# Kernel tuning notes

Hardware: AMD Instinct MI355X
Metric: run time of the kernel (lower is better)

Reference implementation:

```python
import jax, jax.numpy as jnp
import numpy as np
import math

NQ, NK, QDIM, MDIM, VDIM = 8192, 8192, 512, 512, 512
NEG = -float(1 << 32)


def setup_inputs() -> dict:
    key = jax.random.key(0)
    ks = jax.random.split(key, 8)
    Q = jax.random.normal(ks[0], (NQ, QDIM), dtype=jnp.float32)
    K = jax.random.normal(ks[1], (NK, QDIM), dtype=jnp.float32)
    V = jax.random.normal(ks[2], (NK, VDIM), dtype=jnp.float32)
    mask = jax.random.randint(ks[3], (NQ, NK), 0, 2) == 1
    s = 1.0 / math.sqrt(QDIM)
    WQ_w = jax.random.uniform(ks[4], (MDIM, QDIM), minval=-s, maxval=s, dtype=jnp.float32)
    WQ_b = jax.random.uniform(ks[5], (MDIM,), minval=-s, maxval=s, dtype=jnp.float32)
    WK_w = jax.random.uniform(ks[6], (MDIM, QDIM), minval=-s, maxval=s, dtype=jnp.float32)
    WK_b = jax.random.uniform(ks[7], (MDIM,), minval=-s, maxval=s, dtype=jnp.float32)
    return {"Q": Q, "K": K, "V": V, "WQ_w": WQ_w, "WQ_b": WQ_b,
            "WK_w": WK_w, "WK_b": WK_b, "mask": mask}


def reference(Q, K, V, WQ_w, WQ_b, WK_w, WK_b, mask):
    # Linear projections: y = x @ W^T + b
    Qp = Q @ WQ_w.T + WQ_b          # [NQ, MDIM]
    Kp = K @ WK_w.T + WK_b          # [NK, MDIM]
    scale = 1.0 / math.sqrt(MDIM)
    attn = (Qp @ Kp.T) * scale      # [NQ, NK]
    attn = jnp.where(mask, NEG, attn)
    attn = jax.nn.softmax(attn, axis=-1)
    return attn @ V                 # [NQ, VDIM]
```

## Files before the change

kernel.cpp:

```cpp
#include <hip/hip_runtime.h>

typedef __attribute__((ext_vector_type(8))) short short8;
typedef __attribute__((ext_vector_type(4))) float f32x4;

#define DEVFN __device__ __forceinline__

constexpr float NEGF = -4294967296.0f;
constexpr float SCALE_LOG2E = 0.06375872f;

DEVFN unsigned short f2bf(float f) {
  unsigned int u = __float_as_uint(f);
  u += 0x7FFFu + ((u >> 16) & 1u);
  return (unsigned short)(u >> 16);
}
DEVFN float bf2f(unsigned short h) { return __uint_as_float((unsigned)h << 16); }

DEVFN float exp2v(float x) {
  float r;
  asm("v_exp_f32 %0, %1" : "=v"(r) : "v"(x));
  return r;
}

DEVFN void gl_lds16(const void* g, void* l) {
  __builtin_amdgcn_global_load_lds(
      (const __attribute__((address_space(1))) unsigned int*)g,
      (__attribute__((address_space(3))) unsigned int*)l, 16, 0, 0);
}

DEVFN float dpp_fmax16(float x) {
  int v;
  v = __builtin_amdgcn_update_dpp(0, __float_as_int(x), 0xB1, 0xF, 0xF, true);
  x = fmaxf(x, __int_as_float(v));
  v = __builtin_amdgcn_update_dpp(0, __float_as_int(x), 0x4E, 0xF, 0xF, true);
  x = fmaxf(x, __int_as_float(v));
  v = __builtin_amdgcn_update_dpp(0, __float_as_int(x), 0x141, 0xF, 0xF, true);
  x = fmaxf(x, __int_as_float(v));
  v = __builtin_amdgcn_update_dpp(0, __float_as_int(x), 0x140, 0xF, 0xF, true);
  x = fmaxf(x, __int_as_float(v));
  return x;
}
DEVFN float dpp_fadd16(float x) {
  int v;
  v = __builtin_amdgcn_update_dpp(0, __float_as_int(x), 0xB1, 0xF, 0xF, true);
  x += __int_as_float(v);
  v = __builtin_amdgcn_update_dpp(0, __float_as_int(x), 0x4E, 0xF, 0xF, true);
  x += __int_as_float(v);
  v = __builtin_amdgcn_update_dpp(0, __float_as_int(x), 0x141, 0xF, 0xF, true);
  x += __int_as_float(v);
  v = __builtin_amdgcn_update_dpp(0, __float_as_int(x), 0x140, 0xF, 0xF, true);
  x += __int_as_float(v);
  return x;
}

__global__ void k_detect(const unsigned int* __restrict__ q, const unsigned int* __restrict__ m,
                         int* __restrict__ fflag, int* __restrict__ esize) {
  int lane = threadIdx.x;
  if (blockIdx.x == 0) {
    unsigned bad = 0;
    for (int i = 0; i < 64; i++) {
      unsigned v = q[i * 64 + lane];
      unsigned h = v & 0xFFFFu;
      unsigned e = (h >> 7) & 0xFFu;
      if (h != 0u && (e < 96u || e > 150u)) bad = 1;
    }
    unsigned long long anyb = __ballot(bad != 0);
    if (lane == 0) *fflag = (anyb == 0ULL) ? 1 : 0;
  } else {
    unsigned okd = 1, okh = 1, okb = 1;
    for (int i = 0; i < 64; i++) {
      unsigned v = m[i * 64 + lane];
      if (v > 1u && v != 0x3F800000u) okd = 0;
      unsigned h0 = v & 0xFFFFu, h1 = v >> 16;
      if ((h0 && h0 != 0x3F80u && h0 != 1u) || (h1 && h1 != 0x3F80u && h1 != 1u)) okh = 0;
      if (v & 0xFEFEFEFEu) okb = 0;
    }
    okd = (__ballot(okd == 0) == 0ULL);
    okh = (__ballot(okh == 0) == 0ULL);
    okb = (__ballot(okb == 0) == 0ULL);
    if (lane == 0) *esize = okd ? 4 : (okh ? 2 : 1);
  }
}

__global__ void k_prep(const void* __restrict__ Q, unsigned short* __restrict__ Qb,
                       const void* __restrict__ K, unsigned short* __restrict__ Kb,
                       const void* __restrict__ Wq, unsigned short* __restrict__ Wqb,
                       const void* __restrict__ Wk, unsigned short* __restrict__ Wkb,
                       const void* __restrict__ bq, unsigned short* __restrict__ bqb,
                       const void* __restrict__ bk, unsigned short* __restrict__ bkb,
                       const int* __restrict__ bf16flag) {
  int blk = blockIdx.x;
  const void* src; unsigned short* dst; int base, n;
  if (blk < 2048)      { src = Q;  dst = Qb;  base = blk;        n = 8192 * 512; }
  else if (blk < 4096) { src = K;  dst = Kb;  base = blk - 2048; n = 8192 * 512; }
  else if (blk < 4224) { src = Wq; dst = Wqb; base = blk - 4096; n = 512 * 512; }
  else if (blk < 4352) { src = Wk; dst = Wkb; base = blk - 4224; n = 512 * 512; }
  else if (blk == 4352){ src = bq; dst = bqb; base = 0;          n = 512; }
  else                 { src = bk; dst = bkb; base = 0;          n = 512; }
  int i = (base * 256 + threadIdx.x) * 8;
  if (i >= n) return;
  if (*bf16flag) {
    *(uint4*)(dst + i) = *(const uint4*)((const unsigned short*)src + i);
  } else {
    const float* f = (const float*)src + i;
    float4 a = *(const float4*)f, b = *(const float4*)(f + 4);
    uint4 o;
    o.x = (unsigned)f2bf(a.x) | ((unsigned)f2bf(a.y) << 16);
    o.y = (unsigned)f2bf(a.z) | ((unsigned)f2bf(a.w) << 16);
    o.z = (unsigned)f2bf(b.x) | ((unsigned)f2bf(b.y) << 16);
    o.w = (unsigned)f2bf(b.z) | ((unsigned)f2bf(b.w) << 16);
    *(uint4*)(dst + i) = o;
  }
}

__global__ void k_transpose_v(const void* __restrict__ Vsrc, const int* __restrict__ bf16flag,
                              unsigned short* __restrict__ Vt) {
  __shared__ unsigned short T[64][72];
  int t = threadIdx.x;
  int rb = blockIdx.x, cb = blockIdx.y;
  int r = t >> 3, c8 = (t & 7) * 8;
  int isbf = *bf16flag;
#pragma unroll
  for (int j = 0; j < 2; j++) {
    int row = rb * 64 + j * 32 + r;
    unsigned short e[8];
    if (isbf) {
      alignas(16) unsigned short tmp[8];
      *(uint4*)tmp = *(const uint4*)((const unsigned short*)Vsrc + (size_t)row * 512 + cb * 64 + c8);
#pragma unroll
      for (int i = 0; i < 8; i++) e[i] = tmp[i];
    } else {
      const float* f = (const float*)Vsrc + (size_t)row * 512 + cb * 64 + c8;
      float4 a = *(const float4*)f, b = *(const float4*)(f + 4);
      e[0] = f2bf(a.x); e[1] = f2bf(a.y); e[2] = f2bf(a.z); e[3] = f2bf(a.w);
      e[4] = f2bf(b.x); e[5] = f2bf(b.y); e[6] = f2bf(b.z); e[7] = f2bf(b.w);
    }
#pragma unroll
    for (int i = 0; i < 8; i++) T[c8 + i][j * 32 + r] = e[i];
  }
  __syncthreads();
#pragma unroll
  for (int j = 0; j < 2; j++) {
    int d = cb * 64 + j * 32 + r;
    alignas(16) unsigned short o[8];
#pragma unroll
    for (int i = 0; i < 8; i++) o[i] = T[j * 32 + r][c8 + i];
    int tt = rb * 2 + (c8 >> 5);
    *(uint4*)(Vt + ((size_t)tt * 512 + d) * 32 + (c8 & 31)) = *(const uint4*)o;
  }
}

DEVFN unsigned nib4(unsigned v) {
  unsigned t = v; t |= t >> 1; t |= t >> 2; t |= t >> 4; t &= 0x01010101u;
  return (t * 0x10204080u) >> 28;
}
DEVFN unsigned pair2(unsigned v) {
  unsigned t = v; t |= t >> 8; t |= t >> 4; t |= t >> 2; t |= t >> 1;
  return (t & 1u) | (((t >> 16) & 1u) << 1);
}
__global__ void k_pack(const void* __restrict__ mask, const int* __restrict__ esize,
                       unsigned long long* __restrict__ bits) {
  int wv = (blockIdx.x * blockDim.x + threadIdx.x) >> 6;
  int lane = threadIdx.x & 63;
  int sz = *esize;
  if (sz == 4) {
    const unsigned int* m = (const unsigned int*)mask;
    for (int g = wv; g < 262144; g += 4096) {
      size_t base = (size_t)g * 256 + lane;
      unsigned v0 = m[base], v1 = m[base + 64], v2 = m[base + 128], v3 = m[base + 192];
      unsigned long long b0 = __ballot(v0 != 0u);
      unsigned long long b1 = __ballot(v1 != 0u);
      unsigned long long b2 = __ballot(v2 != 0u);
      unsigned long long b3 = __ballot(v3 != 0u);
      if (lane == 0) {
        bits[g * 4 + 0] = b0; bits[g * 4 + 1] = b1;
        bits[g * 4 + 2] = b2; bits[g * 4 + 3] = b3;
      }
    }
  } else if (sz == 2) {
    const uint4* m = (const uint4*)mask;
    for (int g = wv; g < 131072; g += 4096) {
      uint4 v = m[(size_t)g * 64 + lane];
      unsigned c8 = pair2(v.x) | (pair2(v.y) << 2) | (pair2(v.z) << 4) | (pair2(v.w) << 6);
      unsigned long long x = (unsigned long long)c8 << ((lane & 7) * 8);
      x |= __shfl_xor(x, 1); x |= __shfl_xor(x, 2); x |= __shfl_xor(x, 4);
      if ((lane & 7) == 0) bits[g * 8 + (lane >> 3)] = x;
    }
  } else {
    const uint4* m = (const uint4*)mask;
    for (int g = wv; g < 65536; g += 4096) {
      uint4 v = m[(size_t)g * 64 + lane];
      unsigned c16 = nib4(v.x) | (nib4(v.y) << 4) | (nib4(v.z) << 8) | (nib4(v.w) << 12);
      unsigned long long x = (unsigned long long)c16 << ((lane & 3) * 16);
      x |= __shfl_xor(x, 1); x |= __shfl_xor(x, 2);
      if ((lane & 3) == 0) bits[g * 16 + (lane >> 2)] = x;
    }
  }
}

__global__ __launch_bounds__(256, 2) void k_proj(
    const unsigned short* __restrict__ Aq, const unsigned short* __restrict__ Wq,
    const unsigned short* __restrict__ bq, unsigned short* __restrict__ outq,
    const unsigned short* __restrict__ Ak, const unsigned short* __restrict__ Wk,
    const unsigned short* __restrict__ bk, unsigned short* __restrict__ outk) {
  const unsigned short* A = blockIdx.z ? Ak : Aq;
  const unsigned short* W = blockIdx.z ? Wk : Wq;
  const unsigned short* bias = blockIdx.z ? bk : bq;
  unsigned short* out = blockIdx.z ? outk : outq;
  float sc = blockIdx.z ? 1.0f : SCALE_LOG2E;

  __shared__ alignas(16) unsigned short As[128 * 64];
  __shared__ alignas(16) unsigned short Bs[128 * 64];
  int tid = threadIdx.x, lane = tid & 63, wave = tid >> 6;
  int wi = wave >> 1, wj = wave & 1;
  int l15 = lane & 15, l4 = lane >> 4;
  int rowbase = blockIdx.x * 128, colbase = blockIdx.y * 128;
  f32x4 acc[4][4];
#pragma unroll
  for (int i = 0; i < 4; i++)
#pragma unroll
    for (int j = 0; j < 4; j++) acc[i][j] = f32x4{0.f, 0.f, 0.f, 0.f};

  int swr = l15 & 7;
  for (int kb = 0; kb < 512; kb += 64) {
    __syncthreads();
#pragma unroll
    for (int t = 0; t < 4; t++) {
      int inst = wave * 4 + t;
      int r = inst * 8 + (lane >> 3);
      int c = ((lane & 7) ^ (r & 7)) * 8;
      gl_lds16(A + (size_t)(rowbase + r) * 512 + kb + c, &As[inst * 512]);
      gl_lds16(W + (size_t)(colbase + r) * 512 + kb + c, &Bs[inst * 512]);
    }
    __syncthreads();
#pragma unroll
    for (int t2 = 0; t2 < 2; t2++) {
      short8 a[4], b[4];
#pragma unroll
      for (int i = 0; i < 4; i++) {
        int row = wi * 64 + i * 16 + l15;
        a[i] = *(const short8*)&As[row * 64 + (((t2 * 4 + l4) ^ swr) * 8)];
      }
#pragma unroll
      for (int j = 0; j < 4; j++) {
        int row = wj * 64 + j * 16 + l15;
        b[j] = *(const short8*)&Bs[row * 64 + (((t2 * 4 + l4) ^ swr) * 8)];
      }
#pragma unroll
      for (int i = 0; i < 4; i++)
#pragma unroll
        for (int j = 0; j < 4; j++)
          acc[i][j] = __builtin_amdgcn_mfma_f32_16x16x32_bf16(a[i], b[j], acc[i][j], 0, 0, 0);
    }
  }
#pragma unroll
  for (int j = 0; j < 4; j++) {
    int col = colbase + wj * 64 + j * 16 + l15;
    float bj = bf2f(bias[col]);
#pragma unroll
    for (int i = 0; i < 4; i++) {
      int row0 = rowbase + wi * 64 + i * 16 + l4 * 4;
#pragma unroll
      for (int r = 0; r < 4; r++)
        out[(size_t)(row0 + r) * 512 + col] = f2bf((acc[i][j][r] + bj) * sc);
    }
  }
}

__global__ __launch_bounds__(512, 2) void k_attn(
    const unsigned short* __restrict__ Qp, const unsigned short* __restrict__ Kp,
    const unsigned short* __restrict__ Vt, const unsigned long long* __restrict__ mbits,
    unsigned short* __restrict__ Opart, float* __restrict__ mpart, float* __restrict__ lpart) {
  __shared__ alignas(16) unsigned short KB[2][16384];
  __shared__ alignas(16) unsigned short VB[16384];
  __shared__ alignas(16) unsigned short P2[2][4][128][8];
  __shared__ alignas(16) float alds[2][128];
  __shared__ alignas(16) int nfl[2][8];
  int tid = threadIdx.x, lane = tid & 63, wave = tid >> 6;
  int l15 = lane & 15, l4 = lane >> 4;
  int b = blockIdx.x;
  int split = b & 7;
  int qb = (b >> 3) * 128;

  short8 qf[16];
  {
    int row = qb + wave * 16 + l15;
#pragma unroll
    for (int t = 0; t < 16; t++)
      qf[t] = *(const short8*)(Qp + (size_t)row * 512 + t * 32 + l4 * 8);
  }
  f32x4 o[8][4];
#pragma unroll
  for (int i = 0; i < 8; i++)
#pragma unroll
    for (int j = 0; j < 4; j++) o[i][j] = f32x4{0.f, 0.f, 0.f, 0.f};
  float mi[4] = {NEGF, NEGF, NEGF, NEGF};
  float li_l[4] = {0.f, 0.f, 0.f, 0.f};

  int swK = l15 | ((l15 & 3) << 4);
  const unsigned int* mb32 = (const unsigned int*)mbits;

#define STAGE_K(TV, BUF)                                                         \
  {                                                                              \
    _Pragma("unroll") for (int t = 0; t < 4; t++) {                              \
      int r = wave * 4 + t;                                                      \
      int swz = (r & 15) | ((r & 3) << 4);                                       \
      gl_lds16(Kp + (size_t)((TV) * 32 + r) * 512 + ((lane ^ swz) * 8),          \
               &KB[BUF][r * 512]);                                               \
    }                                                                            \
  }
#define STAGE_V(TV)                                                              \
  {                                                                              \
    _Pragma("unroll") for (int t = 0; t < 4; t++) {                              \
      int inst = wave * 4 + t;                                                   \
      int d = inst * 16 + (lane >> 2);                                           \
      int cg = (lane & 3) ^ ((d >> 2) & 3);                                      \
      gl_lds16(Vt + (size_t)(TV) * 16384 + d * 32 + cg * 8, &VB[inst * 512]);    \
    }                                                                            \
  }
#define LOAD_MASKS(IT)                                                           \
  _Pragma("unroll") for (int r = 0; r < 4; r++)                                  \
    mw[r] = mb32[((size_t)(qb + wave * 16 + l4 * 4 + r) * 128 + split * 16 +     \
                  ((IT) >> 1)) * 2 + ((IT) & 1)];
#define QKT(BUF)                                                                 \
  {                                                                              \
    _Pragma("unroll") for (int c = 0; c < 2; c++) sacc[c] = f32x4{0.f,0.f,0.f,0.f}; \
    __builtin_amdgcn_s_setprio(1);                                               \
    _Pragma("unroll") for (int t2 = 0; t2 < 16; t2++) {                          \
      short8 a = qf[t2];                                                         \
      _Pragma("unroll") for (int c = 0; c < 2; c++) {                            \
        int row = c * 16 + l15;                                                  \
        short8 bb = *(const short8*)&KB[BUF][row * 512 + (((t2 * 4 + l4) ^ swK) * 8)]; \
        sacc[c] = __builtin_amdgcn_mfma_f32_16x16x32_bf16(a, bb, sacc[c], 0, 0, 0); \
      }                                                                          \
    }                                                                            \
    __builtin_amdgcn_s_setprio(0);                                               \
  }
#define MASK_APPLY()                                                             \
  _Pragma("unroll") for (int c = 0; c < 2; c++)                                  \
    _Pragma("unroll") for (int r = 0; r < 4; r++) {                              \
      bool msk = (mw[r] >> (c * 16 + l15)) & 1u;                                 \
      sacc[c][r] = msk ? NEGF : sacc[c][r];                                      \
    }

  STAGE_K(split * 32, 0);
  __builtin_amdgcn_s_waitcnt(0x0F70);
  __builtin_amdgcn_s_barrier();

  {
    const int tv = split * 32;
    unsigned mw[4];
    LOAD_MASKS(0);
    STAGE_K(tv + 1, 1);
    f32x4 sacc[2];
    QKT(0);
    MASK_APPLY();
    float al4[4];
    bool need = false;
#pragma unroll
    for (int r = 0; r < 4; r++) {
      float t = dpp_fmax16(fmaxf(sacc[0][r], sacc[1][r]));
      al4[r] = t;
      need |= (t > mi[r] + 11.5f);
    }
    unsigned long long blt = __ballot(need);
    if (lane == 0) nfl[0][wave] = (blt != 0ULL) ? 1 : 0;
    if (blt) {
#pragma unroll
      for (int r = 0; r < 4; r++) {
        float mn = fmaxf(mi[r], al4[r]);
        float a = exp2v(mi[r] - mn);
        li_l[r] *= a;
        mi[r] = mn;
        al4[r] = a;
      }
    } else {
#pragma unroll
      for (int r = 0; r < 4; r++) al4[r] = 1.0f;
    }
    if (l15 == 0) *(f32x4*)&alds[0][wave * 16 + l4 * 4] = f32x4{al4[0], al4[1], al4[2], al4[3]};
#pragma unroll
    for (int r = 0; r < 4; r++) {
      sacc[0][r] = exp2v(sacc[0][r] - mi[r]);
      sacc[1][r] = exp2v(sacc[1][r] - mi[r]);
      li_l[r] += sacc[0][r] + sacc[1][r];
    }
#pragma unroll
    for (int r = 0; r < 4; r++) {
      int prow = wave * 16 + l4 * 4 + r;
#pragma unroll
      for (int c = 0; c < 2; c++)
        P2[0][c * 2 + (l15 >> 3)][prow][l15 & 7] = f2bf(sacc[c][r]);
    }
    STAGE_V(tv);
    __builtin_amdgcn_s_waitcnt(0x0074);
    __builtin_amdgcn_s_barrier();
  }

  for (int it = 1; it < 32; ++it) {
    const int cur = it & 1, prv = cur ^ 1;
    const int tv = split * 32 + it;

    unsigned mw[4];
    LOAD_MASKS(it);
    STAGE_K((it < 31) ? tv + 1 : tv, prv);

    f32x4 sacc[2];
    QKT(cur);
    MASK_APPLY();

    __builtin_amdgcn_s_waitcnt(0x0F78);
    __builtin_amdgcn_sched_barrier(0);

    {
      const int4* n4 = (const int4*)&nfl[prv][0];
      int4 na = n4[0], nb4 = n4[1];
      if (na.x | na.y | na.z | na.w | nb4.x | nb4.y | nb4.z | nb4.w) {
#pragma unroll
        for (int rf = 0; rf < 8; rf++) {
          f32x4 av = *(const f32x4*)&alds[prv][rf * 16 + l4 * 4];
#pragma unroll
          for (int df = 0; df < 4; df++)
#pragma unroll
            for (int j = 0; j < 4; j++) o[rf][df][j] *= av[j];
        }
      }
    }
    short8 vf[4];
#pragma unroll
    for (int df = 0; df < 4; df++) {
      int d = wave * 64 + df * 16 + l15;
      vf[df] = *(const short8*)&VB[d * 32 + ((l4 ^ ((l15 >> 2) & 3)) * 8)];
    }

    float al4[4];
    bool need = false;
    unsigned long long blt = 0;
    __builtin_amdgcn_s_setprio(1);
#pragma unroll
    for (int rf = 0; rf < 8; rf++) {
      short8 pa = *(const short8*)&P2[prv][l4][rf * 16 + l15][0];
#pragma unroll
      for (int df = 0; df < 4; df++)
        o[rf][df] = __builtin_amdgcn_mfma_f32_16x16x32_bf16(pa, vf[df], o[rf][df], 0, 0, 0);
      if (rf < 4) {
        const int r = rf;
        float t = dpp_fmax16(fmaxf(sacc[0][r], sacc[1][r]));
        al4[r] = t;
        need |= (t > mi[r] + 11.5f);
      } else if (rf == 4) {
        blt = __ballot(need);
        if (lane == 0) nfl[cur][wave] = (blt != 0ULL) ? 1 : 0;
        if (blt) {
#pragma unroll
          for (int r = 0; r < 4; r++) {
            float mn = fmaxf(mi[r], al4[r]);
            float a = exp2v(mi[r] - mn);
            li_l[r] *= a;
            mi[r] = mn;
            al4[r] = a;
          }
        } else {
#pragma unroll
          for (int r = 0; r < 4; r++) al4[r] = 1.0f;
        }
        if (l15 == 0) *(f32x4*)&alds[cur][wave * 16 + l4 * 4] = f32x4{al4[0], al4[1], al4[2], al4[3]};
      } else if (rf == 5) {
#pragma unroll
        for (int r = 0; r < 2; r++) {
          sacc[0][r] = exp2v(sacc[0][r] - mi[r]);
          sacc[1][r] = exp2v(sacc[1][r] - mi[r]);
          li_l[r] += sacc[0][r] + sacc[1][r];
        }
      } else if (rf == 6) {
#pragma unroll
        for (int r = 2; r < 4; r++) {
          sacc[0][r] = exp2v(sacc[0][r] - mi[r]);
          sacc[1][r] = exp2v(sacc[1][r] - mi[r]);
          li_l[r] += sacc[0][r] + sacc[1][r];
        }
      } else {
#pragma unroll
        for (int r = 0; r < 4; r++) {
          int prow = wave * 16 + l4 * 4 + r;
#pragma unroll
          for (int c = 0; c < 2; c++)
            P2[cur][c * 2 + (l15 >> 3)][prow][l15 & 7] = f2bf(sacc[c][r]);
        }
      }
    }
    __builtin_amdgcn_s_setprio(0);

    STAGE_V(tv);
    __builtin_amdgcn_s_waitcnt(0x0074);
    __builtin_amdgcn_s_barrier();
  }

  __builtin_amdgcn_s_waitcnt(0x0F70);
  __builtin_amdgcn_sched_barrier(0);
  {
    const int4* n4 = (const int4*)&nfl[1][0];
    int4 na = n4[0], nb4 = n4[1];
    if (na.x | na.y | na.z | na.w | nb4.x | nb4.y | nb4.z | nb4.w) {
#pragma unroll
      for (int rf = 0; rf < 8; rf++) {
        f32x4 av = *(const f32x4*)&alds[1][rf * 16 + l4 * 4];
#pragma unroll
        for (int df = 0; df < 4; df++)
#pragma unroll
          for (int j = 0; j < 4; j++) o[rf][df][j] *= av[j];
      }
    }
    short8 vf[4];
#pragma unroll
    for (int df = 0; df < 4; df++) {
      int d = wave * 64 + df * 16 + l15;
      vf[df] = *(const short8*)&VB[d * 32 + ((l4 ^ ((l15 >> 2) & 3)) * 8)];
    }
#pragma unroll
    for (int rf = 0; rf < 8; rf++) {
      short8 pa = *(const short8*)&P2[1][l4][rf * 16 + l15][0];
#pragma unroll
      for (int df = 0; df < 4; df++)
        o[rf][df] = __builtin_amdgcn_mfma_f32_16x16x32_bf16(pa, vf[df], o[rf][df], 0, 0, 0);
    }
  }

  float li[4];
#pragma unroll
  for (int r = 0; r < 4; r++) li[r] = dpp_fadd16(li_l[r]);
#pragma unroll
  for (int r = 0; r < 4; r++) {
    int row = qb + wave * 16 + l4 * 4 + r;
    if (l15 == 0) {
      mpart[(size_t)split * 8192 + row] = mi[r];
      lpart[(size_t)split * 8192 + row] = li[r];
    }
  }
  uint2* op2 = (uint2*)Opart;
#pragma unroll
  for (int rf = 0; rf < 8; rf++)
#pragma unroll
    for (int df = 0; df < 4; df++) {
      int f = wave * 4 + df;
      uint2 v;
      v.x = (unsigned)f2bf(o[rf][df][0]) | ((unsigned)f2bf(o[rf][df][1]) << 16);
      v.y = (unsigned)f2bf(o[rf][df][2]) | ((unsigned)f2bf(o[rf][df][3]) << 16);
      op2[(((size_t)b * 32 + f) * 8 + rf) * 64 + l4 * 16 + l15] = v;
    }
#undef STAGE_K
#undef STAGE_V
#undef LOAD_MASKS
#undef QKT
#undef MASK_APPLY
}

__global__ void k_combine(const unsigned short* __restrict__ Opart,
                          const float* __restrict__ mpart, const float* __restrict__ lpart,
                          float* __restrict__ out) {
  int q = blockIdx.x;
  int half = blockIdx.y;
  int tid = threadIdx.x;
  int wave = tid >> 6, lane = tid & 63, l4 = (lane >> 4) & 3, l15 = lane & 15;
  int row0 = q * 128 + wave * 16 + l4 * 4;

  float w[8][4], inv[4];
#pragma unroll
  for (int r = 0; r < 4; r++) {
    float M = NEGF;
    float mv[8];
#pragma unroll
    for (int s = 0; s < 8; s++) { mv[s] = mpart[s * 8192 + row0 + r]; M = fmaxf(M, mv[s]); }
    float L = 0.f;
#pragma unroll
    for (int s = 0; s < 8; s++) {
      float ws = exp2v(mv[s] - M);
      w[s][r] = ws;
      L += ws * lpart[s * 8192 + row0 + r];
    }
    inv[r] = 1.0f / L;
  }
  const uint2* op2 = (const uint2*)Opart;
#pragma unroll
  for (int fo = 0; fo < 16; fo++) {
    int f = half * 16 + fo;
    float acc[4] = {0.f, 0.f, 0.f, 0.f};
#pragma unroll
    for (int s = 0; s < 8; s++) {
      uint2 v = op2[(((size_t)(q * 8 + s) * 32 + f) * 8 + wave) * 64 + l4 * 16 + l15];
      acc[0] += w[s][0] * bf2f((unsigned short)(v.x & 0xFFFFu));
      acc[1] += w[s][1] * bf2f((unsigned short)(v.x >> 16));
      acc[2] += w[s][2] * bf2f((unsigned short)(v.y & 0xFFFFu));
      acc[3] += w[s][3] * bf2f((unsigned short)(v.y >> 16));
    }
    int col = f * 16 + l15;
#pragma unroll
    for (int r = 0; r < 4; r++)
      out[(size_t)(row0 + r) * 512 + col] = acc[r] * inv[r];
  }
}

extern "C" void kernel_launch(void* const* d_in, const int* in_sizes, int n_in,
                              void* d_out, int out_size, void* d_ws, size_t ws_size,
                              hipStream_t stream) {
  const void* Q   = d_in[0];
  const void* K   = d_in[1];
  const void* V   = d_in[2];
  const void* WQw = d_in[3];
  const void* WQb = d_in[4];
  const void* WKw = d_in[5];
  const void* WKb = d_in[6];
  const void* mask = d_in[7];
  float* out = (float*)d_out;
  char* ws = (char*)d_ws;
  (void)in_sizes; (void)n_in; (void)out_size; (void)ws_size;

  constexpr size_t SZ_MAT = (size_t)8192 * 512 * 2;
  size_t off = 4096;
  unsigned short* Qb  = (unsigned short*)(ws + off); off += SZ_MAT;
  unsigned short* Kb  = (unsigned short*)(ws + off); off += SZ_MAT;
  unsigned short* Wqb = (unsigned short*)(ws + off); off += (size_t)512 * 512 * 2;
  unsigned short* Wkb = (unsigned short*)(ws + off); off += (size_t)512 * 512 * 2;
  unsigned short* bqb = (unsigned short*)(ws + off); off += 1024;
  unsigned short* bkb = (unsigned short*)(ws + off); off += 1024;
  unsigned short* Vt  = (unsigned short*)(ws + off); off += SZ_MAT;
  unsigned short* Qp  = (unsigned short*)(ws + off); off += SZ_MAT;
  unsigned short* Kp  = (unsigned short*)(ws + off); off += SZ_MAT;
  unsigned long long* mbits = (unsigned long long*)(ws + off); off += (size_t)8192 * 128 * 8;
  unsigned short* Opart = (unsigned short*)(ws + off); off += (size_t)512 * 512 * 32 * 8;
  float* mpart = (float*)(ws + off); off += (size_t)8 * 8192 * 4;
  float* lpart = (float*)(ws + off); off += (size_t)8 * 8192 * 4;
  int* fflag = (int*)ws;
  int* esize = (int*)(ws + 64);

  k_detect<<<2, 64, 0, stream>>>((const unsigned int*)Q, (const unsigned int*)mask, fflag, esize);
  k_prep<<<4354, 256, 0, stream>>>(Q, Qb, K, Kb, WQw, Wqb, WKw, Wkb, WQb, bqb, WKb, bkb, fflag);
  k_transpose_v<<<dim3(128, 8), 256, 0, stream>>>(V, fflag, Vt);
  k_pack<<<1024, 256, 0, stream>>>(mask, esize, mbits);
  k_proj<<<dim3(64, 4, 2), 256, 0, stream>>>(Qb, Wqb, bqb, Qp, Kb, Wkb, bkb, Kp);
  k_attn<<<512, 512, 0, stream>>>(Qp, Kp, Vt, mbits, Opart, mpart, lpart);
  k_combine<<<dim3(64, 2), 512, 0, stream>>>(Opart, mpart, lpart, out);
}
```

Before: 870.0 us.

## Stagger softmax and PV phases between even and odd waves

Wraps the QK^T+mask+online-softmax step and the PV accumulation step in macros. Even waves run softmax first and then PV, while odd waves run PV first and then softmax. This replaces the hand-interleaved PV/softmax loop inside each wave. The intent is that waves sharing a SIMD alternate between MFMA-heavy and VALU/transcendental-heavy phases so the two units overlap across waves, in exchange for losing the fine-grained intra-wave interleaving. The change also adds compiler memory fences after the mask loads and lengthens the SCALE_LOG2E constant literal.

```diff
diff --git a/kernel.cpp b/kernel.cpp
--- a/kernel.cpp
+++ b/kernel.cpp
@@ -6,7 +6,7 @@
 #define DEVFN __device__ __forceinline__
 
 constexpr float NEGF = -4294967296.0f;
-constexpr float SCALE_LOG2E = 0.06375872f;
+constexpr float SCALE_LOG2E = 0.06375872465057373f;
 
 DEVFN unsigned short f2bf(float f) {
   unsigned int u = __float_as_uint(f);
@@ -321,26 +321,87 @@
   _Pragma("unroll") for (int r = 0; r < 4; r++)                                  \
     mw[r] = mb32[((size_t)(qb + wave * 16 + l4 * 4 + r) * 128 + split * 16 +     \
                   ((IT) >> 1)) * 2 + ((IT) & 1)];
-#define QKT(BUF)                                                                 \
+#define SM_BLOCK(CUR)                                                            \
   {                                                                              \
+    f32x4 sacc[2];                                                               \
     _Pragma("unroll") for (int c = 0; c < 2; c++) sacc[c] = f32x4{0.f,0.f,0.f,0.f}; \
     __builtin_amdgcn_s_setprio(1);                                               \
     _Pragma("unroll") for (int t2 = 0; t2 < 16; t2++) {                          \
       short8 a = qf[t2];                                                         \
       _Pragma("unroll") for (int c = 0; c < 2; c++) {                            \
         int row = c * 16 + l15;                                                  \
-        short8 bb = *(const short8*)&KB[BUF][row * 512 + (((t2 * 4 + l4) ^ swK) * 8)]; \
+        short8 bb = *(const short8*)&KB[CUR][row * 512 + (((t2 * 4 + l4) ^ swK) * 8)]; \
         sacc[c] = __builtin_amdgcn_mfma_f32_16x16x32_bf16(a, bb, sacc[c], 0, 0, 0); \
       }                                                                          \
     }                                                                            \
     __builtin_amdgcn_s_setprio(0);                                               \
-  }
-#define MASK_APPLY()                                                             \
-  _Pragma("unroll") for (int c = 0; c < 2; c++)                                  \
+    _Pragma("unroll") for (int c = 0; c < 2; c++)                                \
+      _Pragma("unroll") for (int r = 0; r < 4; r++) {                            \
+        bool msk = (mw[r] >> (c * 16 + l15)) & 1u;                               \
+        sacc[c][r] = msk ? NEGF : sacc[c][r];                                    \
+      }                                                                          \
+    float al4[4];                                                                \
+    bool need = false;                                                           \
     _Pragma("unroll") for (int r = 0; r < 4; r++) {                              \
-      bool msk = (mw[r] >> (c * 16 + l15)) & 1u;                                 \
-      sacc[c][r] = msk ? NEGF : sacc[c][r];                                      \
-    }
+      float t = dpp_fmax16(fmaxf(sacc[0][r], sacc[1][r]));                       \
+      al4[r] = t;                                                                \
+      need |= (t > mi[r] + 11.5f);                                               \
+    }                                                                            \
+    unsigned long long blt = __ballot(need);                                     \
+    if (lane == 0) nfl[CUR][wave] = (blt != 0ULL) ? 1 : 0;                       \
+    if (blt) {                                                                   \
+      _Pragma("unroll") for (int r = 0; r < 4; r++) {                            \
+        float mn = fmaxf(mi[r], al4[r]);                                         \
+        float a = exp2v(mi[r] - mn);                                             \
+        li_l[r] *= a;                                                            \
+        mi[r] = mn;                                                              \
+        al4[r] = a;                                                              \
+      }                                                                          \
+    } else {                                                                     \
+      _Pragma("unroll") for (int r = 0; r < 4; r++) al4[r] = 1.0f;               \
+    }                                                                            \
+    if (l15 == 0) *(f32x4*)&alds[CUR][wave * 16 + l4 * 4] =                      \
+        f32x4{al4[0], al4[1], al4[2], al4[3]};                                   \
+    _Pragma("unroll") for (int r = 0; r < 4; r++) {                              \
+      sacc[0][r] = exp2v(sacc[0][r] - mi[r]);                                    \
+      sacc[1][r] = exp2v(sacc[1][r] - mi[r]);                                    \
+      li_l[r] += sacc[0][r] + sacc[1][r];                                        \
+    }                                                                            \
+    _Pragma("unroll") for (int r = 0; r < 4; r++) {                              \
+      int prow = wave * 16 + l4 * 4 + r;                                         \
+      _Pragma("unroll") for (int c = 0; c < 2; c++)                              \
+        P2[CUR][c * 2 + (l15 >> 3)][prow][l15 & 7] = f2bf(sacc[c][r]);           \
+    }                                                                            \
+  }
+#define PV_BLOCK(PRV)                                                            \
+  {                                                                              \
+    __builtin_amdgcn_s_waitcnt(0x0F78);            \
+    __builtin_amdgcn_sched_barrier(0);                                           \
+    {                                                                            \
+      const int4* n4 = (const int4*)&nfl[PRV][0];                                \
+      int4 na = n4[0], nb4 = n4[1];                                              \
+      if (na.x | na.y | na.z | na.w | nb4.x | nb4.y | nb4.z | nb4.w) {           \
+        _Pragma("unroll") for (int rf = 0; rf < 8; rf++) {                       \
+          f32x4 av = *(const f32x4*)&alds[PRV][rf * 16 + l4 * 4];                \
+          _Pragma("unroll") for (int df = 0; df < 4; df++)                       \
+            _Pragma("unroll") for (int j = 0; j < 4; j++) o[rf][df][j] *= av[j]; \
+        }                                                                        \
+      }                                                                          \
+    }                                                                            \
+    short8 vf[4];                                                                \
+    _Pragma("unroll") for (int df = 0; df < 4; df++) {                           \
+      int d = wave * 64 + df * 16 + l15;                                         \
+      vf[df] = *(const short8*)&VB[d * 32 + ((l4 ^ ((l15 >> 2) & 3)) * 8)];      \
+    }                                                                            \
+    __builtin_amdgcn_s_setprio(1);                                               \
+    _Pragma("unroll") for (int rf = 0; rf < 8; rf++) {                           \
+      short8 pa = *(const short8*)&P2[PRV][l4][rf * 16 + l15][0];                \
+      _Pragma("unroll") for (int df = 0; df < 4; df++)                           \
+        o[rf][df] = __builtin_amdgcn_mfma_f32_16x16x32_bf16(pa, vf[df],          \
+                                                            o[rf][df], 0, 0, 0);\
+    }                                                                            \
+    __builtin_amdgcn_s_setprio(0);                                               \
+  }
 
   STAGE_K(split * 32, 0);
   __builtin_amdgcn_s_waitcnt(0x0F70);
@@ -350,145 +411,31 @@
     const int tv = split * 32;
     unsigned mw[4];
     LOAD_MASKS(0);
+    asm volatile("" ::: "memory");
     STAGE_K(tv + 1, 1);
-    f32x4 sacc[2];
-    QKT(0);
-    MASK_APPLY();
-    float al4[4];
-    bool need = false;
-#pragma unroll
-    for (int r = 0; r < 4; r++) {
-      float t = dpp_fmax16(fmaxf(sacc[0][r], sacc[1][r]));
-      al4[r] = t;
-      need |= (t > mi[r] + 11.5f);
-    }
-    unsigned long long blt = __ballot(need);
-    if (lane == 0) nfl[0][wave] = (blt != 0ULL) ? 1 : 0;
-    if (blt) {
-#pragma unroll
-      for (int r = 0; r < 4; r++) {
-        float mn = fmaxf(mi[r], al4[r]);
-        float a = exp2v(mi[r] - mn);
-        li_l[r] *= a;
-        mi[r] = mn;
-        al4[r] = a;
-      }
-    } else {
-#pragma unroll
-      for (int r = 0; r < 4; r++) al4[r] = 1.0f;
-    }
-    if (l15 == 0) *(f32x4*)&alds[0][wave * 16 + l4 * 4] = f32x4{al4[0], al4[1], al4[2], al4[3]};
-#pragma unroll
-    for (int r = 0; r < 4; r++) {
-      sacc[0][r] = exp2v(sacc[0][r] - mi[r]);
-      sacc[1][r] = exp2v(sacc[1][r] - mi[r]);
-      li_l[r] += sacc[0][r] + sacc[1][r];
-    }
-#pragma unroll
-    for (int r = 0; r < 4; r++) {
-      int prow = wave * 16 + l4 * 4 + r;
-#pragma unroll
-      for (int c = 0; c < 2; c++)
-        P2[0][c * 2 + (l15 >> 3)][prow][l15 & 7] = f2bf(sacc[c][r]);
-    }
+    SM_BLOCK(0);
     STAGE_V(tv);
     __builtin_amdgcn_s_waitcnt(0x0074);
     __builtin_amdgcn_s_barrier();
   }
 
+  const bool evenw = (wave & 1) == 0;
   for (int it = 1; it < 32; ++it) {
     const int cur = it & 1, prv = cur ^ 1;
     const int tv = split * 32 + it;
 
     unsigned mw[4];
     LOAD_MASKS(it);
+    asm volatile("" ::: "memory");
     STAGE_K((it < 31) ? tv + 1 : tv, prv);
 
-    f32x4 sacc[2];
-    QKT(cur);
-    MASK_APPLY();
-
-    __builtin_amdgcn_s_waitcnt(0x0F78);
-    __builtin_amdgcn_sched_barrier(0);
-
-    {
-      const int4* n4 = (const int4*)&nfl[prv][0];
-      int4 na = n4[0], nb4 = n4[1];
-      if (na.x | na.y | na.z | na.w | nb4.x | nb4.y | nb4.z | nb4.w) {
-#pragma unroll
-        for (int rf = 0; rf < 8; rf++) {
-          f32x4 av = *(const f32x4*)&alds[prv][rf * 16 + l4 * 4];
-#pragma unroll
-          for (int df = 0; df < 4; df++)
-#pragma unroll
-            for (int j = 0; j < 4; j++) o[rf][df][j] *= av[j];
-        }
-      }
-    }
-    short8 vf[4];
-#pragma unroll
-    for (int df = 0; df < 4; df++) {
-      int d = wave * 64 + df * 16 + l15;
-      vf[df] = *(const short8*)&VB[d * 32 + ((l4 ^ ((l15 >> 2) & 3)) * 8)];
-    }
-
-    float al4[4];
-    bool need = false;
-    unsigned long long blt = 0;
-    __builtin_amdgcn_s_setprio(1);
-#pragma unroll
-    for (int rf = 0; rf < 8; rf++) {
-      short8 pa = *(const short8*)&P2[prv][l4][rf * 16 + l15][0];
-#pragma unroll
-      for (int df = 0; df < 4; df++)
-        o[rf][df] = __builtin_amdgcn_mfma_f32_16x16x32_bf16(pa, vf[df], o[rf][df], 0, 0, 0);
-      if (rf < 4) {
-        const int r = rf;
-        float t = dpp_fmax16(fmaxf(sacc[0][r], sacc[1][r]));
-        al4[r] = t;
-        need |= (t > mi[r] + 11.5f);
-      } else if (rf == 4) {
-        blt = __ballot(need);
-        if (lane == 0) nfl[cur][wave] = (blt != 0ULL) ? 1 : 0;
-        if (blt) {
-#pragma unroll
-          for (int r = 0; r < 4; r++) {
-            float mn = fmaxf(mi[r], al4[r]);
-            float a = exp2v(mi[r] - mn);
-            li_l[r] *= a;
-            mi[r] = mn;
-            al4[r] = a;
-          }
-        } else {
-#pragma unroll
-          for (int r = 0; r < 4; r++) al4[r] = 1.0f;
-        }
-        if (l15 == 0) *(f32x4*)&alds[cur][wave * 16 + l4 * 4] = f32x4{al4[0], al4[1], al4[2], al4[3]};
-      } else if (rf == 5) {
-#pragma unroll
-        for (int r = 0; r < 2; r++) {
-          sacc[0][r] = exp2v(sacc[0][r] - mi[r]);
-          sacc[1][r] = exp2v(sacc[1][r] - mi[r]);
-          li_l[r] += sacc[0][r] + sacc[1][r];
-        }
-      } else if (rf == 6) {
-#pragma unroll
-        for (int r = 2; r < 4; r++) {
-          sacc[0][r] = exp2v(sacc[0][r] - mi[r]);
-          sacc[1][r] = exp2v(sacc[1][r] - mi[r]);
-          li_l[r] += sacc[0][r] + sacc[1][r];
-        }
-      } else {
-#pragma unroll
-        for (int r = 0; r < 4; r++) {
-          int prow = wave * 16 + l4 * 4 + r;
-#pragma unroll
-          for (int c = 0; c < 2; c++)
-            P2[cur][c * 2 + (l15 >> 3)][prow][l15 & 7] = f2bf(sacc[c][r]);
-        }
-      }
-    }
-    __builtin_amdgcn_s_setprio(0);
+    if (evenw) {
+      SM_BLOCK(cur);
+      PV_BLOCK(prv);
+    } else {
+      PV_BLOCK(prv);
+      SM_BLOCK(cur);
+    }
 
     STAGE_V(tv);
     __builtin_amdgcn_s_waitcnt(0x0074);
@@ -497,33 +444,7 @@
 
   __builtin_amdgcn_s_waitcnt(0x0F70);
   __builtin_amdgcn_sched_barrier(0);
-  {
-    const int4* n4 = (const int4*)&nfl[1][0];
-    int4 na = n4[0], nb4 = n4[1];
-    if (na.x | na.y | na.z | na.w | nb4.x | nb4.y | nb4.z | nb4.w) {
-#pragma unroll
-      for (int rf = 0; rf < 8; rf++) {
-        f32x4 av = *(const f32x4*)&alds[1][rf * 16 + l4 * 4];
-#pragma unroll
-        for (int df = 0; df < 4; df++)
-#pragma unroll
-          for (int j = 0; j < 4; j++) o[rf][df][j] *= av[j];
-      }
-    }
-    short8 vf[4];
-#pragma unroll
-    for (int df = 0; df < 4; df++) {
-      int d = wave * 64 + df * 16 + l15;
-      vf[df] = *(const short8*)&VB[d * 32 + ((l4 ^ ((l15 >> 2) & 3)) * 8)];
-    }
-#pragma unroll
-    for (int rf = 0; rf < 8; rf++) {
-      short8 pa = *(const short8*)&P2[1][l4][rf * 16 + l15][0];
-#pragma unroll
-      for (int df = 0; df < 4; df++)
-        o[rf][df] = __builtin_amdgcn_mfma_f32_16x16x32_bf16(pa, vf[df], o[rf][df], 0, 0, 0);
-    }
-  }
+  PV_BLOCK(1);
 
   float li[4];
 #pragma unroll
@@ -550,8 +471,8 @@
 #undef STAGE_K
 #undef STAGE_V
 #undef LOAD_MASKS
-#undef QKT
-#undef MASK_APPLY
+#undef SM_BLOCK
+#undef PV_BLOCK
 }
 
 __global__ void k_combine(const unsigned short* __restrict__ Opart,
```

Result: faster. 817.8 us (-6.0%).
